# Optimization experiments

Hardware: AMD Instinct MI355X
Metric: run time of the kernel (lower is better)

The kernel has to match this reference:

```python
import jax, jax.numpy as jnp
import numpy as np

B, T, C = 8, 2048, 512
KEY_SIZE, VALUE_SIZE = 512, 512


def setup_inputs() -> dict:
    key = jax.random.key(0)
    ks = jax.random.split(key, 7)
    s = 0.02
    return {
        "input": jax.random.normal(ks[0], (B, T, C), dtype=jnp.float32),
        "Wq": jax.random.normal(ks[1], (KEY_SIZE, C), dtype=jnp.float32) * s,
        "bq": jax.random.normal(ks[2], (KEY_SIZE,), dtype=jnp.float32) * s,
        "Wk": jax.random.normal(ks[3], (KEY_SIZE, C), dtype=jnp.float32) * s,
        "bk": jax.random.normal(ks[4], (KEY_SIZE,), dtype=jnp.float32) * s,
        "Wv": jax.random.normal(ks[5], (VALUE_SIZE, C), dtype=jnp.float32) * s,
        "bv": jax.random.normal(ks[6], (VALUE_SIZE,), dtype=jnp.float32) * s,
    }


def reference(input, Wq, bq, Wk, bk, Wv, bv):
    # input: [B, T, C]
    sqrt_key_size = jnp.sqrt(jnp.float32(Wq.shape[0]))
    query = jnp.einsum('btc,kc->btk', input, Wq) + bq   # [B, T, K]
    keys = jnp.einsum('btc,kc->btk', input, Wk) + bk    # [B, T, K]
    values = jnp.einsum('btc,vc->btv', input, Wv) + bv  # [B, T, V]
    # logits[b, j, i] = q_j . k_i
    logits = jnp.einsum('bjk,bik->bji', query, keys)    # [B, T, T]
    # mask[j, i] = True where i > j (future key positions) -> -inf
    j = jnp.arange(logits.shape[1])[:, None]
    i = jnp.arange(logits.shape[2])[None, :]
    mask = i > j
    masked = jnp.where(mask[None, :, :], -jnp.inf, logits)
    # NOTE: original softmaxes over dim=1 (the query axis), non-standard.
    probs = jax.nn.softmax(masked / sqrt_key_size, axis=1)  # [B, T, T]
    read = jnp.einsum('bji,biv->bjv', probs, values)        # [B, T, V]
    return jnp.concatenate((input, read), axis=2)           # [B, T, C+V]
```

## Files before the change

### kernel.cpp

```cpp
#include <hip/hip_runtime.h>

typedef unsigned short u16;
using bf16x8 = __attribute__((ext_vector_type(8))) short;
using f32x4  = __attribute__((ext_vector_type(4))) float;

static __device__ __forceinline__ u16 f2b(float f) {
  unsigned int x = __builtin_bit_cast(unsigned int, f);
  unsigned int r = (x + 0x7fffu + ((x >> 16) & 1u)) >> 16;
  return (u16)r;
}
static __device__ __forceinline__ float fin(float x) { return (x != x) ? 0.f : x; }
static __device__ __forceinline__ float expclamp(float x) {
  return __expf(fminf(fmaxf(x, -80.f), 80.f));
}
static __device__ __forceinline__ unsigned cvt2(float lo, float hi) {
  unsigned r;
  asm("v_cvt_pk_bf16_f32 %0, %1, %2" : "=v"(r) : "v"(lo), "v"(hi));
  return r;
}

#define SCALE 0.04419417382415922f
#define MFMA16(a, b, c) __builtin_amdgcn_mfma_f32_16x16x32_bf16((a), (b), (c), 0, 0, 0)

static __device__ __forceinline__ void glds16(const u16* g, u16* l) {
  __builtin_amdgcn_global_load_lds(
      (const __attribute__((address_space(1))) unsigned int*)(unsigned long long)(const void*)g,
      (__attribute__((address_space(3))) unsigned int*)(unsigned int)(unsigned long long)(void*)l,
      16, 0, 0);
}


__global__ __launch_bounds__(256) void qkv_mfma(
    const float* __restrict__ X,
    const float* __restrict__ Wq, const float* __restrict__ bq,
    const float* __restrict__ Wk, const float* __restrict__ bk,
    const float* __restrict__ Wv, const float* __restrict__ bv,
    u16* __restrict__ outq, u16* __restrict__ Kw, u16* __restrict__ Vt) {
  __shared__ __align__(16) u16 SM[16384];
  u16* As = SM;
  u16* Bs = SM + 8192;
  const int id = blockIdx.x;
  const int xcd = id & 7;
  const int slot = id >> 3;
  const int bxl = slot / 12;
  const int byz = slot - bxl * 12;
  const int z = byz >> 2;
  const int by = byz & 3;
  const int bx = (xcd << 4) + bxl;
  const float* W = (z == 0) ? Wq : ((z == 1) ? Wk : Wv);
  const float* bias = (z == 0) ? bq : ((z == 1) ? bk : bv);
  const int row0 = bx * 128;
  const int col0 = by * 128;
  const int tid = threadIdx.x, lane = tid & 63, w = tid >> 6;
  const int lrow = lane & 15, lg = lane >> 4;
  const int qm = w >> 1, qn = w & 1;
  const int srow = tid >> 1, sh = tid & 1;

  const f32x4 Z4 = {0.f, 0.f, 0.f, 0.f};
  f32x4 acc[4][4];
#pragma unroll
  for (int m = 0; m < 4; ++m)
#pragma unroll
    for (int n = 0; n < 4; ++n) acc[m][n] = Z4;

  const float* Xr = X + (size_t)(row0 + srow) * 512;
  const float* Wr = W + (size_t)(col0 + srow) * 512;

  for (int ks = 0; ks < 8; ++ks) {
    const int k0 = ks * 64;
    __syncthreads();
#pragma unroll
    for (int s4 = 0; s4 < 4; ++s4) {
      const int slt = sh * 4 + s4;
      const int ds = ((slt ^ (srow & 7)) << 3);
      {
        float4 f0 = *(const float4*)(Xr + k0 + slt * 8);
        float4 f1 = *(const float4*)(Xr + k0 + slt * 8 + 4);
        uint4 pk;
        pk.x = cvt2(f0.x, f0.y); pk.y = cvt2(f0.z, f0.w);
        pk.z = cvt2(f1.x, f1.y); pk.w = cvt2(f1.z, f1.w);
        *(uint4*)&As[srow * 64 + ds] = pk;
      }
      {
        float4 f0 = *(const float4*)(Wr + k0 + slt * 8);
        float4 f1 = *(const float4*)(Wr + k0 + slt * 8 + 4);
        uint4 pk;
        pk.x = cvt2(f0.x, f0.y); pk.y = cvt2(f0.z, f0.w);
        pk.z = cvt2(f1.x, f1.y); pk.w = cvt2(f1.z, f1.w);
        *(uint4*)&Bs[srow * 64 + ds] = pk;
      }
    }
    __syncthreads();
#pragma unroll
    for (int cs = 0; cs < 2; ++cs) {
      bf16x8 af[4], bfr[4];
#pragma unroll
      for (int mf = 0; mf < 4; ++mf) {
        const int r = qm * 64 + mf * 16 + lrow;
        af[mf] = *(const bf16x8*)&As[r * 64 + (((cs * 4 + lg) ^ (r & 7)) << 3)];
      }
#pragma unroll
      for (int nf = 0; nf < 4; ++nf) {
        const int r = qn * 64 + nf * 16 + lrow;
        bfr[nf] = *(const bf16x8*)&Bs[r * 64 + (((cs * 4 + lg) ^ (r & 7)) << 3)];
      }
#pragma unroll
      for (int mf = 0; mf < 4; ++mf)
#pragma unroll
        for (int nf = 0; nf < 4; ++nf)
          acc[mf][nf] = MFMA16(af[mf], bfr[nf], acc[mf][nf]);
    }
  }

  if (z < 2) {
    u16* O = (z == 0) ? outq : Kw;
    const int ldo = (z == 0) ? 2048 : 512;
#pragma unroll
    for (int mf = 0; mf < 4; ++mf)
#pragma unroll
      for (int nf = 0; nf < 4; ++nf) {
        const int C = col0 + qn * 64 + nf * 16 + lrow;
        const float bb = bias[C];
#pragma unroll
        for (int r = 0; r < 4; ++r) {
          const int R = row0 + qm * 64 + mf * 16 + lg * 4 + r;
          O[(size_t)R * ldo + C] = f2b(fin(acc[mf][nf][r] + bb));
        }
      }
  } else {
    __syncthreads();
    u16* Tr = SM;
#pragma unroll
    for (int mf = 0; mf < 4; ++mf)
#pragma unroll
      for (int nf = 0; nf < 4; ++nf) {
        const int vl = qn * 64 + nf * 16 + lrow;
        const float bb = bias[col0 + vl];
#pragma unroll
        for (int r = 0; r < 4; ++r) {
          const int tl = qm * 64 + mf * 16 + lg * 4 + r;
          Tr[vl * 128 + tl] = f2b(fin(acc[mf][nf][r] + bb));
        }
      }
    __syncthreads();
    const int vl = tid >> 1, part = tid & 1;
    const int bI = row0 >> 11;
    u16* dst = Vt + (size_t)(bI * 512 + col0 + vl) * 2048 + (row0 & 2047) + part * 64;
    const u16* sp = &Tr[vl * 128 + part * 64];
#pragma unroll
    for (int q = 0; q < 8; ++q)
      *(uint4*)(dst + q * 8) = *(const uint4*)(sp + q * 8);
  }
}

__global__ __launch_bounds__(512, 4) void denom_mfma(
    const u16* __restrict__ Qs, const u16* __restrict__ Kw, float* __restrict__ rdn) {
  __shared__ __align__(16) u16 QB[2][16384];
  __shared__ float red[4][2][16];
  const int id = blockIdx.x;
  const int b = id & 7, rest = id >> 3;
  const int py = rest >> 2, stripe = rest & 3;
  const int tid = threadIdx.x, lane = tid & 63, w = tid >> 6;
  const int lrow = lane & 15, lg = lane >> 4;
  const int ihh = w >> 1, jq = w & 1;
  const size_t kbase = (size_t)b * 2048 * 512;
  const f32x4 Z4 = {0.f, 0.f, 0.f, 0.f};

  for (int pass = 0; pass < 2; ++pass) {
    const int ti = pass ? (31 - py) : py;
    const int i0 = ti * 64;
    bf16x8 Kf[16];
    const u16* kr = Kw + kbase + (size_t)(i0 + ihh * 16 + lrow) * 512;
#pragma unroll
    for (int cs = 0; cs < 16; ++cs) Kf[cs] = *(const bf16x8*)(kr + cs * 32 + lg * 8);
    float dacc[4] = {0.f, 0.f, 0.f, 0.f};
    const int m0 = (i0 >> 5) + stripe;

    if (m0 <= 63) {
#pragma unroll
      for (int p = 0; p < 4; ++p) {
        const int row = p * 8 + w;
        glds16(Qs + (size_t)(b * 2048 + m0 * 32 + row) * 2048 + ((lane ^ (row & 7)) << 3),
               &QB[0][row * 512]);
      }
    }
    __syncthreads();

    int n = 0;
    for (int m = m0; m <= 63; m += 4, ++n) {
      const int cur = n & 1;
      if (m + 4 <= 63) {
#pragma unroll
        for (int p = 0; p < 4; ++p) {
          const int row = p * 8 + w;
          glds16(Qs + (size_t)(b * 2048 + (m + 4) * 32 + row) * 2048 + ((lane ^ (row & 7)) << 3),
                 &QB[cur ^ 1][row * 512]);
        }
      }
      const u16* qb = &QB[cur][0];
      const int qrow = jq * 16 + lrow;
      f32x4 sA = Z4, sB = Z4;
#pragma unroll
      for (int cs = 0; cs < 8; ++cs) {
        bf16x8 q0 = *(const bf16x8*)(qb + qrow * 512 + (((cs * 4 + lg) ^ (lrow & 7)) << 3));
        bf16x8 q1 = *(const bf16x8*)(qb + qrow * 512 + (((32 + cs * 4 + lg) ^ (lrow & 7)) << 3));
        sA = MFMA16(Kf[cs], q0, sA);
        sB = MFMA16(Kf[cs + 8], q1, sB);
      }
      const int jG = m * 32 + jq * 16 + lrow;
      const int ib = i0 + ihh * 16 + lg * 4;
#pragma unroll
      for (int r = 0; r < 4; ++r) {
        float e = (jG >= ib + r) ? expclamp((sA[r] + sB[r]) * SCALE) : 0.f;
        e += __shfl_xor(e, 1); e += __shfl_xor(e, 2);
        e += __shfl_xor(e, 4); e += __shfl_xor(e, 8);
        dacc[r] += e;
      }
      __syncthreads();
    }

    if (lrow == 0) {
#pragma unroll
      for (int r = 0; r < 4; ++r) red[ihh][jq][lg * 4 + r] = dacc[r];
    }
    __syncthreads();
    if (tid < 64) {
      const float d = red[tid >> 4][0][tid & 15] + red[tid >> 4][1][tid & 15];
      rdn[(size_t)(b * 2048 + i0 + tid) * 1024 + 256 + stripe] = d;
    }
    __syncthreads();
  }
}

__global__ __launch_bounds__(512, 4) void read_mfma(
    const u16* __restrict__ Qs, const u16* __restrict__ Kw, const u16* __restrict__ Vt,
    const float* __restrict__ rdn, float* __restrict__ outf) {
  __shared__ __align__(16) u16 KB[2][16384];
  __shared__ __align__(16) u16 PB[2][32 * 40];
  const int id = blockIdx.x;
  const int b = id & 7, s = id >> 3;
  const int jt = (s < 32) ? s : 95 - s;
  const int j0 = jt * 32;
  const int tid = threadIdx.x, lane = tid & 63, w = tid >> 6;
  const int lrow = lane & 15, lg = lane >> 4;
  const int role = w >> 2, wq = w & 3;
  const int jh = wq >> 1, iq = wq & 1;
  const int vq = wq;
  const int NW = jt + 1;
  const size_t kbase = (size_t)b * 2048 * 512;
  const size_t vbase = (size_t)b * 512 * 2048;
  const f32x4 Z4 = {0.f, 0.f, 0.f, 0.f};

  f32x4 RS[16];
  if (role == 0) {
    const u16* qr = Qs + (size_t)(b * 2048 + j0 + jh * 16 + lrow) * 2048;
#pragma unroll
    for (int cs = 0; cs < 16; ++cs)
      RS[cs] = __builtin_bit_cast(f32x4, *(const bf16x8*)(qr + cs * 32 + lg * 8));
  } else {
#pragma unroll
    for (int t = 0; t < 16; ++t) RS[t] = Z4;
  }

#pragma unroll
  for (int p = 0; p < 4; ++p) {
    const int row = p * 8 + w;
    glds16(Kw + kbase + (size_t)row * 512 + ((lane ^ (row & 7)) << 3),
           &KB[0][row * 512]);
  }
  __syncthreads();

  for (int t = 0; t <= NW; ++t) {
    if (t + 1 < NW) {
#pragma unroll
      for (int p = 0; p < 4; ++p) {
        const int row = p * 8 + w;
        glds16(Kw + kbase + (size_t)((t + 1) * 32 + row) * 512 + ((lane ^ (row & 7)) << 3),
               &KB[(t + 1) & 1][row * 512]);
      }
    }
    if (role == 0) {
      if (t < NW) {
        const int i0 = t * 32;
        const int iG = i0 + iq * 16 + lrow;
        const float4 rp = *(const float4*)&rdn[(size_t)(b * 2048 + iG) * 1024 + 256];
        const u16* kb = &KB[t & 1][0];
        const int krow = iq * 16 + lrow;
        f32x4 sA = Z4, sB = Z4;
#pragma unroll
        for (int cs = 0; cs < 8; ++cs) {
          bf16x8 k0 = *(const bf16x8*)(kb + krow * 512 + (((cs * 4 + lg) ^ (lrow & 7)) << 3));
          bf16x8 k1 = *(const bf16x8*)(kb + krow * 512 + (((32 + cs * 4 + lg) ^ (lrow & 7)) << 3));
          sA = MFMA16(__builtin_bit_cast(bf16x8, RS[cs]), k0, sA);
          sB = MFMA16(__builtin_bit_cast(bf16x8, RS[cs + 8]), k1, sB);
        }
        const float rd = 1.0f / fmaxf(rp.x + rp.y + rp.z + rp.w, 1e-30f);
        const int jb = j0 + jh * 16 + lg * 4;
#pragma unroll
        for (int r = 0; r < 4; ++r) {
          const float e = (iG <= jb + r) ? expclamp((sA[r] + sB[r]) * SCALE) * rd : 0.f;
          PB[t & 1][(jh * 16 + lg * 4 + r) * 40 + iq * 16 + lrow] = f2b(e);
        }
      }
    } else {
      if (t >= 1) {
        const int i0 = (t - 1) * 32;
        bf16x8 Vp[8];
#pragma unroll
        for (int vt = 0; vt < 8; ++vt)
          Vp[vt] = *(const bf16x8*)(
              Vt + vbase + (size_t)(vq * 128 + vt * 16 + lrow) * 2048 + i0 + lg * 8);
        const u16* pb = &PB[(t - 1) & 1][0];
        const bf16x8 pa0 = *(const bf16x8*)(pb + lrow * 40 + lg * 8);
        const bf16x8 pa1 = *(const bf16x8*)(pb + (16 + lrow) * 40 + lg * 8);
#pragma unroll
        for (int vt = 0; vt < 8; ++vt) {
          RS[vt] = MFMA16(pa0, Vp[vt], RS[vt]);
          RS[8 + vt] = MFMA16(pa1, Vp[vt], RS[8 + vt]);
        }
      }
    }
    __syncthreads();
  }

  if (role == 1) {
#pragma unroll
    for (int jh2 = 0; jh2 < 2; ++jh2)
#pragma unroll
      for (int vt = 0; vt < 8; ++vt) {
        const int v = vq * 128 + vt * 16 + lrow;
        const f32x4 o = RS[jh2 * 8 + vt];
#pragma unroll
        for (int r = 0; r < 4; ++r) {
          const int jj = j0 + jh2 * 16 + lg * 4 + r;
          outf[(size_t)(b * 2048 + jj) * 1024 + 512 + v] = fin(o[r]);
        }
      }
  }
}

__global__ __launch_bounds__(256) void copy_in_kernel(
    const float* __restrict__ X, float* __restrict__ outf) {
  size_t idx = (size_t)blockIdx.x * 256 + threadIdx.x;
  size_t row = idx >> 7;
  int c = (int)(idx & 127) * 4;
  *(float4*)&outf[row * 1024 + c] = *(const float4*)&X[row * 512 + c];
}

extern "C" void kernel_launch(void* const* d_in, const int* in_sizes, int n_in,
                              void* d_out, int out_size, void* d_ws, size_t ws_size,
                              hipStream_t stream) {
  const float* X  = (const float*)d_in[0];
  const float* Wq = (const float*)d_in[1];
  const float* bq = (const float*)d_in[2];
  const float* Wk = (const float*)d_in[3];
  const float* bk = (const float*)d_in[4];
  const float* Wv = (const float*)d_in[5];
  const float* bv = (const float*)d_in[6];

  char* ws = (char*)d_ws;
  const size_t SZ = (size_t)16384 * 512 * sizeof(u16);
  u16* Kw = (u16*)(ws);
  u16* Vt = (u16*)(ws + SZ);

  qkv_mfma<<<dim3(1536), 256, 0, stream>>>(X, Wq, bq, Wk, bk, Wv, bv,
                                           (u16*)d_out, Kw, Vt);
  denom_mfma<<<dim3(512), 512, 0, stream>>>((const u16*)d_out, Kw, (float*)d_out);
  read_mfma<<<dim3(512), 512, 0, stream>>>((const u16*)d_out, Kw, Vt,
                                           (const float*)d_out, (float*)d_out);
  copy_in_kernel<<<8192, 256, 0, stream>>>(X, (float*)d_out);
}
```

Baseline: 381.4 us.

## Load Q and K tiles directly from global memory instead of LDS double buffering

In both the denominator and read kernels, the global_load_lds double-buffered staging of Q/K tiles in shared memory is removed. Each lane now loads its MFMA operand fragments straight from global memory into registers, relying on cache reuse. The denominator kernel also drops its per-iteration barrier and moves the cross-lane shuffle reduction out of the loop. This frees a large amount of LDS and removes barriers, but gives up the explicit prefetch overlap and may raise global/L2 traffic and exposed load latency.

```diff
diff --git a/kernel.cpp b/kernel.cpp
--- a/kernel.cpp
+++ b/kernel.cpp
@@ -21,13 +21,6 @@
 
 #define SCALE 0.04419417382415922f
 #define MFMA16(a, b, c) __builtin_amdgcn_mfma_f32_16x16x32_bf16((a), (b), (c), 0, 0, 0)
-
-static __device__ __forceinline__ void glds16(const u16* g, u16* l) {
-  __builtin_amdgcn_global_load_lds(
-      (const __attribute__((address_space(1))) unsigned int*)(unsigned long long)(const void*)g,
-      (__attribute__((address_space(3))) unsigned int*)(unsigned int)(unsigned long long)(void*)l,
-      16, 0, 0);
-}
 
 
 __global__ __launch_bounds__(256) void qkv_mfma(
@@ -155,7 +148,6 @@
 
 __global__ __launch_bounds__(512, 4) void denom_mfma(
     const u16* __restrict__ Qs, const u16* __restrict__ Kw, float* __restrict__ rdn) {
-  __shared__ __align__(16) u16 QB[2][16384];
   __shared__ float red[4][2][16];
   const int id = blockIdx.x;
   const int b = id & 7, rest = id >> 3;
@@ -176,52 +168,31 @@
     float dacc[4] = {0.f, 0.f, 0.f, 0.f};
     const int m0 = (i0 >> 5) + stripe;
 
-    if (m0 <= 63) {
-#pragma unroll
-      for (int p = 0; p < 4; ++p) {
-        const int row = p * 8 + w;
-        glds16(Qs + (size_t)(b * 2048 + m0 * 32 + row) * 2048 + ((lane ^ (row & 7)) << 3),
-               &QB[0][row * 512]);
-      }
-    }
-    __syncthreads();
-
-    int n = 0;
-    for (int m = m0; m <= 63; m += 4, ++n) {
-      const int cur = n & 1;
-      if (m + 4 <= 63) {
-#pragma unroll
-        for (int p = 0; p < 4; ++p) {
-          const int row = p * 8 + w;
-          glds16(Qs + (size_t)(b * 2048 + (m + 4) * 32 + row) * 2048 + ((lane ^ (row & 7)) << 3),
-                 &QB[cur ^ 1][row * 512]);
-        }
-      }
-      const u16* qb = &QB[cur][0];
-      const int qrow = jq * 16 + lrow;
+    for (int m = m0; m <= 63; m += 4) {
+      const u16* qr = Qs + (size_t)(b * 2048 + m * 32 + jq * 16 + lrow) * 2048;
       f32x4 sA = Z4, sB = Z4;
-#pragma unroll
-      for (int cs = 0; cs < 8; ++cs) {
-        bf16x8 q0 = *(const bf16x8*)(qb + qrow * 512 + (((cs * 4 + lg) ^ (lrow & 7)) << 3));
-        bf16x8 q1 = *(const bf16x8*)(qb + qrow * 512 + (((32 + cs * 4 + lg) ^ (lrow & 7)) << 3));
-        sA = MFMA16(Kf[cs], q0, sA);
-        sB = MFMA16(Kf[cs + 8], q1, sB);
-      }
+      bf16x8 qf[8];
+#pragma unroll
+      for (int cs = 0; cs < 8; ++cs) qf[cs] = *(const bf16x8*)(qr + cs * 32 + lg * 8);
+#pragma unroll
+      for (int cs = 0; cs < 8; ++cs) sA = MFMA16(Kf[cs], qf[cs], sA);
+#pragma unroll
+      for (int cs = 0; cs < 8; ++cs) qf[cs] = *(const bf16x8*)(qr + (cs + 8) * 32 + lg * 8);
+#pragma unroll
+      for (int cs = 0; cs < 8; ++cs) sB = MFMA16(Kf[cs + 8], qf[cs], sB);
       const int jG = m * 32 + jq * 16 + lrow;
       const int ib = i0 + ihh * 16 + lg * 4;
 #pragma unroll
-      for (int r = 0; r < 4; ++r) {
-        float e = (jG >= ib + r) ? expclamp((sA[r] + sB[r]) * SCALE) : 0.f;
-        e += __shfl_xor(e, 1); e += __shfl_xor(e, 2);
-        e += __shfl_xor(e, 4); e += __shfl_xor(e, 8);
-        dacc[r] += e;
-      }
-      __syncthreads();
-    }
-
-    if (lrow == 0) {
-#pragma unroll
-      for (int r = 0; r < 4; ++r) red[ihh][jq][lg * 4 + r] = dacc[r];
+      for (int r = 0; r < 4; ++r)
+        dacc[r] += (jG >= ib + r) ? expclamp((sA[r] + sB[r]) * SCALE) : 0.f;
+    }
+
+#pragma unroll
+    for (int r = 0; r < 4; ++r) {
+      float v = dacc[r];
+      v += __shfl_xor(v, 1); v += __shfl_xor(v, 2);
+      v += __shfl_xor(v, 4); v += __shfl_xor(v, 8);
+      if (lrow == 0) red[ihh][jq][lg * 4 + r] = v;
     }
     __syncthreads();
     if (tid < 64) {
@@ -235,7 +206,6 @@
 __global__ __launch_bounds__(512, 4) void read_mfma(
     const u16* __restrict__ Qs, const u16* __restrict__ Kw, const u16* __restrict__ Vt,
     const float* __restrict__ rdn, float* __restrict__ outf) {
-  __shared__ __align__(16) u16 KB[2][16384];
   __shared__ __align__(16) u16 PB[2][32 * 40];
   const int id = blockIdx.x;
   const int b = id & 7, s = id >> 3;
@@ -262,38 +232,25 @@
     for (int t = 0; t < 16; ++t) RS[t] = Z4;
   }
 
-#pragma unroll
-  for (int p = 0; p < 4; ++p) {
-    const int row = p * 8 + w;
-    glds16(Kw + kbase + (size_t)row * 512 + ((lane ^ (row & 7)) << 3),
-           &KB[0][row * 512]);
-  }
-  __syncthreads();
-
   for (int t = 0; t <= NW; ++t) {
-    if (t + 1 < NW) {
-#pragma unroll
-      for (int p = 0; p < 4; ++p) {
-        const int row = p * 8 + w;
-        glds16(Kw + kbase + (size_t)((t + 1) * 32 + row) * 512 + ((lane ^ (row & 7)) << 3),
-               &KB[(t + 1) & 1][row * 512]);
-      }
-    }
     if (role == 0) {
       if (t < NW) {
         const int i0 = t * 32;
         const int iG = i0 + iq * 16 + lrow;
         const float4 rp = *(const float4*)&rdn[(size_t)(b * 2048 + iG) * 1024 + 256];
-        const u16* kb = &KB[t & 1][0];
-        const int krow = iq * 16 + lrow;
+        const u16* kr = Kw + kbase + (size_t)iG * 512;
         f32x4 sA = Z4, sB = Z4;
-#pragma unroll
-        for (int cs = 0; cs < 8; ++cs) {
-          bf16x8 k0 = *(const bf16x8*)(kb + krow * 512 + (((cs * 4 + lg) ^ (lrow & 7)) << 3));
-          bf16x8 k1 = *(const bf16x8*)(kb + krow * 512 + (((32 + cs * 4 + lg) ^ (lrow & 7)) << 3));
-          sA = MFMA16(__builtin_bit_cast(bf16x8, RS[cs]), k0, sA);
-          sB = MFMA16(__builtin_bit_cast(bf16x8, RS[cs + 8]), k1, sB);
-        }
+        bf16x8 kf[8];
+#pragma unroll
+        for (int cs = 0; cs < 8; ++cs) kf[cs] = *(const bf16x8*)(kr + cs * 32 + lg * 8);
+#pragma unroll
+        for (int cs = 0; cs < 8; ++cs)
+          sA = MFMA16(__builtin_bit_cast(bf16x8, RS[cs]), kf[cs], sA);
+#pragma unroll
+        for (int cs = 0; cs < 8; ++cs) kf[cs] = *(const bf16x8*)(kr + (cs + 8) * 32 + lg * 8);
+#pragma unroll
+        for (int cs = 0; cs < 8; ++cs)
+          sB = MFMA16(__builtin_bit_cast(bf16x8, RS[cs + 8]), kf[cs], sB);
         const float rd = 1.0f / fmaxf(rp.x + rp.y + rp.z + rp.w, 1e-30f);
         const int jb = j0 + jh * 16 + lg * 4;
 #pragma unroll
```

Result: slower. 554.6 us (+45.4%).

## Batch LDS loads before MFMA chains, defer shuffle reduction, reorder block scheduling

Applied to the files above, without the earlier changes.

The denominator kernel's inner loop now accumulates per-lane exp values and runs the cross-lane shuffle reduction once after the loop, instead of doing it on every iteration. In both kernels, the LDS fragment loads are grouped into batches of eight ahead of each MFMA chain so load latency is hidden. The read kernel now maps block ids so the longest causal tiles (high jt) are dispatched first, which should improve tail load balance. The batched loads raise register pressure, which could lower occupancy.

```diff
diff --git a/kernel.cpp b/kernel.cpp
--- a/kernel.cpp
+++ b/kernel.cpp
@@ -200,28 +200,31 @@
       const u16* qb = &QB[cur][0];
       const int qrow = jq * 16 + lrow;
       f32x4 sA = Z4, sB = Z4;
-#pragma unroll
-      for (int cs = 0; cs < 8; ++cs) {
-        bf16x8 q0 = *(const bf16x8*)(qb + qrow * 512 + (((cs * 4 + lg) ^ (lrow & 7)) << 3));
-        bf16x8 q1 = *(const bf16x8*)(qb + qrow * 512 + (((32 + cs * 4 + lg) ^ (lrow & 7)) << 3));
-        sA = MFMA16(Kf[cs], q0, sA);
-        sB = MFMA16(Kf[cs + 8], q1, sB);
-      }
+      bf16x8 qf[8];
+#pragma unroll
+      for (int cs = 0; cs < 8; ++cs)
+        qf[cs] = *(const bf16x8*)(qb + qrow * 512 + (((cs * 4 + lg) ^ (lrow & 7)) << 3));
+#pragma unroll
+      for (int cs = 0; cs < 8; ++cs) sA = MFMA16(Kf[cs], qf[cs], sA);
+#pragma unroll
+      for (int cs = 0; cs < 8; ++cs)
+        qf[cs] = *(const bf16x8*)(qb + qrow * 512 + ((((cs + 8) * 4 + lg) ^ (lrow & 7)) << 3));
+#pragma unroll
+      for (int cs = 0; cs < 8; ++cs) sB = MFMA16(Kf[cs + 8], qf[cs], sB);
       const int jG = m * 32 + jq * 16 + lrow;
       const int ib = i0 + ihh * 16 + lg * 4;
 #pragma unroll
-      for (int r = 0; r < 4; ++r) {
-        float e = (jG >= ib + r) ? expclamp((sA[r] + sB[r]) * SCALE) : 0.f;
-        e += __shfl_xor(e, 1); e += __shfl_xor(e, 2);
-        e += __shfl_xor(e, 4); e += __shfl_xor(e, 8);
-        dacc[r] += e;
-      }
+      for (int r = 0; r < 4; ++r)
+        dacc[r] += (jG >= ib + r) ? expclamp((sA[r] + sB[r]) * SCALE) : 0.f;
       __syncthreads();
     }
 
-    if (lrow == 0) {
-#pragma unroll
-      for (int r = 0; r < 4; ++r) red[ihh][jq][lg * 4 + r] = dacc[r];
+#pragma unroll
+    for (int r = 0; r < 4; ++r) {
+      float v = dacc[r];
+      v += __shfl_xor(v, 1); v += __shfl_xor(v, 2);
+      v += __shfl_xor(v, 4); v += __shfl_xor(v, 8);
+      if (lrow == 0) red[ihh][jq][lg * 4 + r] = v;
     }
     __syncthreads();
     if (tid < 64) {
@@ -238,8 +241,8 @@
   __shared__ __align__(16) u16 KB[2][16384];
   __shared__ __align__(16) u16 PB[2][32 * 40];
   const int id = blockIdx.x;
-  const int b = id & 7, s = id >> 3;
-  const int jt = (s < 32) ? s : 95 - s;
+  const int b = id & 7, k = id >> 3;
+  const int jt = (k < 32) ? (63 - k) : (k - 32);
   const int j0 = jt * 32;
   const int tid = threadIdx.x, lane = tid & 63, w = tid >> 6;
   const int lrow = lane & 15, lg = lane >> 4;
@@ -287,13 +290,19 @@
         const u16* kb = &KB[t & 1][0];
         const int krow = iq * 16 + lrow;
         f32x4 sA = Z4, sB = Z4;
-#pragma unroll
-        for (int cs = 0; cs < 8; ++cs) {
-          bf16x8 k0 = *(const bf16x8*)(kb + krow * 512 + (((cs * 4 + lg) ^ (lrow & 7)) << 3));
-          bf16x8 k1 = *(const bf16x8*)(kb + krow * 512 + (((32 + cs * 4 + lg) ^ (lrow & 7)) << 3));
-          sA = MFMA16(__builtin_bit_cast(bf16x8, RS[cs]), k0, sA);
-          sB = MFMA16(__builtin_bit_cast(bf16x8, RS[cs + 8]), k1, sB);
-        }
+        bf16x8 kf[8];
+#pragma unroll
+        for (int cs = 0; cs < 8; ++cs)
+          kf[cs] = *(const bf16x8*)(kb + krow * 512 + (((cs * 4 + lg) ^ (lrow & 7)) << 3));
+#pragma unroll
+        for (int cs = 0; cs < 8; ++cs)
+          sA = MFMA16(__builtin_bit_cast(bf16x8, RS[cs]), kf[cs], sA);
+#pragma unroll
+        for (int cs = 0; cs < 8; ++cs)
+          kf[cs] = *(const bf16x8*)(kb + krow * 512 + (((32 + cs * 4 + lg) ^ (lrow & 7)) << 3));
+#pragma unroll
+        for (int cs = 0; cs < 8; ++cs)
+          sB = MFMA16(__builtin_bit_cast(bf16x8, RS[cs + 8]), kf[cs], sB);
         const float rd = 1.0f / fmaxf(rp.x + rp.y + rp.z + rp.w, 1e-30f);
         const int jb = j0 + jh * 16 + lg * 4;
 #pragma unroll
```

After: 373.4 us. 1.02x faster.
